# Performance work log

Hardware: AMD Instinct MI355X
Metric: run time of the kernel (lower is better)

## Reference

```python
import jax, jax.numpy as jnp
import numpy as np
from jax import lax

B, C_IN, C_OUT, K, N_W, L = 32, 256, 256, 7, 8, 4096
SQ = C_IN // 32  # squeezed dim = 8
STRIDE, PAD = 1, 3


def setup_inputs() -> dict:
    key = jax.random.key(0)
    ks = jax.random.split(key, 8)
    s = 0.05
    return {
        "x": jax.random.normal(ks[0], (B, C_IN, L), dtype=jnp.float32),
        "conv_weight": jax.random.normal(ks[1], (C_OUT, C_IN, K, N_W), dtype=jnp.float32) * s,
        "w1": jax.random.normal(ks[2], (C_IN, SQ), dtype=jnp.float32) * s,   # linear1 weight (x @ w1)
        "b1": jax.random.normal(ks[3], (SQ,), dtype=jnp.float32) * s,
        "wk": jax.random.normal(ks[4], (SQ, K), dtype=jnp.float32) * s,      # kernel head
        "wi": jax.random.normal(ks[5], (SQ, C_IN), dtype=jnp.float32) * s,   # inc head
        "wo": jax.random.normal(ks[6], (SQ, C_OUT), dtype=jnp.float32) * s,  # outc head
        "wn": jax.random.normal(ks[7], (SQ, N_W), dtype=jnp.float32) * s,    # nums head
    }


def reference(x, conv_weight, w1, b1, wk, wi, wo, wn):
    # SqueezeFeedForward: AdaptiveAvgPool1d(1) == mean over length, then Linear + exact GELU
    pooled = jnp.mean(x, axis=-1)                        # [B, C_in]
    h = jax.nn.gelu(pooled @ w1 + b1, approximate=False)  # [B, SQ]

    kr = jax.nn.sigmoid(h @ wk)          # [B, K]
    inc = jax.nn.sigmoid(h @ wi)         # [B, C_in]
    outc = jax.nn.sigmoid(h @ wo)        # [B, C_out]
    nums = jax.nn.softmax(h @ wn, -1)    # [B, N_w]

    # Per-sample mixed weights: sum over num_weight of 4-way outer-product gated base weight
    w = jnp.einsum('bk,bi,bo,bn,oikn->boik', kr, inc, outc, nums, conv_weight)  # [B,O,I,K]

    b, o, i, k = w.shape
    l = x.shape[-1]
    # Batched per-sample conv via grouped conv: groups = B
    lhs = x.reshape(1, b * i, l)         # [1, B*I, L]
    rhs = w.reshape(b * o, i, k)         # [B*O, I, K]
    out = lax.conv_general_dilated(
        lhs, rhs,
        window_strides=(STRIDE,),
        padding=[(PAD, PAD)],
        dimension_numbers=('NCH', 'OIH', 'NCH'),
        feature_group_count=b,
    )
    return out.reshape(b, o, -1)         # [B, O, L_out]
```

## Files before the change

### kernel.cpp

```cpp
#include <hip/hip_runtime.h>
#include <hip/hip_bf16.h>
#include <math.h>

#define B_   32
#define CI   256
#define CO   256
#define KW   7
#define NW   8
#define SQD  8
#define L_   4096

typedef __attribute__((ext_vector_type(8))) __bf16 bf16x8;
typedef __attribute__((ext_vector_type(4))) __bf16 bf16x4;
typedef __attribute__((ext_vector_type(4))) float  f32x4;

static __device__ __forceinline__ unsigned short f2bf(float f) {
    unsigned int u = __builtin_bit_cast(unsigned int, f);
    u += 0x7FFFu + ((u >> 16) & 1u);
    return (unsigned short)(u >> 16);
}
static __device__ __forceinline__ uint2 pack4bf(float a, float b, float c, float d) {
    bf16x4 v;
    v[0] = (__bf16)a; v[1] = (__bf16)b; v[2] = (__bf16)c; v[3] = (__bf16)d;
    return __builtin_bit_cast(uint2, v);
}

__global__ __launch_bounds__(256) void k1_mean(
        const float* __restrict__ x, float* __restrict__ pooled) {
    int row = blockIdx.x;
    const float* p = x + (size_t)row * L_;
    int t = threadIdx.x;
    float s = 0.f;
#pragma unroll
    for (int it = 0; it < 4; ++it) {
        float4 v = *(const float4*)(p + (size_t)(t + 256 * it) * 4);
        s += v.x + v.y + v.z + v.w;
    }
    for (int m = 1; m <= 32; m <<= 1) s += __shfl_xor(s, m);
    __shared__ float wsum[4];
    if ((t & 63) == 0) wsum[t >> 6] = s;
    __syncthreads();
    if (t == 0)
        pooled[row] = (wsum[0] + wsum[1] + wsum[2] + wsum[3]) * (1.0f / L_);
}

__global__ __launch_bounds__(64) void k2_gates(
        const float* __restrict__ pooled,
        const float* __restrict__ w1, const float* __restrict__ b1,
        const float* __restrict__ wk, const float* __restrict__ wi,
        const float* __restrict__ wo, const float* __restrict__ wn,
        float* __restrict__ kr, float* __restrict__ inc,
        float* __restrict__ outc, float* __restrict__ nums)
{
    int b = blockIdx.x, lane = threadIdx.x;
    float pc[4];
#pragma unroll
    for (int j = 0; j < 4; ++j)
        pc[j] = pooled[b * CI + lane + 64 * j];
    float h[SQD];
#pragma unroll
    for (int s = 0; s < SQD; ++s) {
        float ps = 0.f;
#pragma unroll
        for (int j = 0; j < 4; ++j)
            ps += pc[j] * w1[(lane + 64 * j) * SQD + s];
        for (int m = 1; m <= 32; m <<= 1) ps += __shfl_xor(ps, m);
        float z = ps + b1[s];
        h[s] = 0.5f * z * (1.0f + erff(z * 0.70710678118654752f));
    }
    if (lane < KW) {
        float a = 0.f;
#pragma unroll
        for (int s = 0; s < SQD; ++s) a += h[s] * wk[s * KW + lane];
        kr[b * 8 + lane] = 1.0f / (1.0f + expf(-a));
    }
    if (lane < NW) {
        float e[NW]; float mx = -1e30f;
#pragma unroll
        for (int n = 0; n < NW; ++n) {
            float a = 0.f;
#pragma unroll
            for (int s = 0; s < SQD; ++s) a += h[s] * wn[s * NW + n];
            e[n] = a; mx = fmaxf(mx, a);
        }
        float den = 0.f;
#pragma unroll
        for (int n = 0; n < NW; ++n) den += expf(e[n] - mx);
        nums[b * NW + lane] = expf(e[lane] - mx) / den;
    }
#pragma unroll
    for (int j = 0; j < 4; ++j) {
        int c = lane + 64 * j;
        float a = 0.f, o2 = 0.f;
#pragma unroll
        for (int s = 0; s < SQD; ++s) {
            a  += h[s] * wi[s * CI + c];
            o2 += h[s] * wo[s * CO + c];
        }
        inc[b * CI + c]  = 1.0f / (1.0f + expf(-a));
        outc[b * CO + c] = 1.0f / (1.0f + expf(-o2));
    }
}

__global__ __launch_bounds__(256) void k3_wgen(
        const float* __restrict__ cw,
        const float* __restrict__ kr, const float* __restrict__ inc,
        const float* __restrict__ outc, const float* __restrict__ nums,
        unsigned short* __restrict__ W2) {
    __shared__ float s_nums[B_][NW];
    __shared__ float s_kr[B_][KW];
    __shared__ float s_inc[B_][32];
    __shared__ float s_outc[B_][8];
    int t = threadIdx.x;
    int ic = blockIdx.x & 7, o0 = (blockIdx.x >> 3) * 8;
    s_nums[t >> 3][t & 7] = nums[t];
    if (t < B_ * KW) s_kr[t / KW][t % KW] = kr[(t / KW) * 8 + (t % KW)];
    for (int u = t; u < 32 * 32; u += 256) {
        int bb = u >> 5, ii = u & 31;
        s_inc[bb][ii] = inc[bb * CI + ic * 32 + ii];
    }
    for (int u = t; u < 32 * 8; u += 256) {
        int bb = u >> 3, oo = u & 7;
        s_outc[bb][oo] = outc[bb * CO + o0 + oo];
    }
    __syncthreads();
    int ii = t & 31, oo = t >> 5;
    int o = o0 + oo, i = ic * 32 + ii;
    float cwv[KW][NW];
    const float* p = cw + ((size_t)(o * CI + i)) * (KW * NW);
#pragma unroll
    for (int k = 0; k < KW; ++k)
#pragma unroll
        for (int n = 0; n < NW; ++n) cwv[k][n] = p[k * NW + n];
    for (int bb = 0; bb < B_; ++bb) {
        float gio = s_inc[bb][ii] * s_outc[bb][oo];
#pragma unroll
        for (int k = 0; k < KW; ++k) {
            float sk = 0.f;
#pragma unroll
            for (int n = 0; n < NW; ++n) sk += s_nums[bb][n] * cwv[k][n];
            float w = s_kr[bb][k] * gio * sk;
            W2[(((size_t)(bb * KW + k) * 8 + ic) * CO + o) * 32 + ii] = f2bf(w);
        }
    }
}

__global__ __launch_bounds__(1024) void k4_conv(
        const float* __restrict__ x,
        const unsigned short* __restrict__ W2,
        float* __restrict__ out) {
    __shared__ __align__(16) unsigned short xs[262 * 264];
    int bid = blockIdx.x;
    int wg  = (bid & 7) * 64 + (bid >> 3);
    int b = wg >> 4, l0 = (wg & 15) * 256;
    int t = threadIdx.x;
    const float* xb = x + (size_t)b * CI * L_;

    {
        int P = t >> 4, lam = t & 15;
        int up = P & 31, half = P >> 5;
        int i0 = (up & 7) * 32 + (up >> 3) * 8;
#pragma unroll
        for (int it = 0; it < 2; ++it) {
            int ch = lam + 16 * (half * 2 + it);
            const float* src = xb + (size_t)i0 * L_ + l0 + ch * 4;
            float4 f[8];
#pragma unroll
            for (int e = 0; e < 8; ++e)
                f[e] = *(const float4*)(src + (size_t)e * L_);
#pragma unroll
            for (int j = 0; j < 4; ++j) {
                int r = 4 * ch + j + 3;
                uint2 a = pack4bf((&f[0].x)[j], (&f[1].x)[j], (&f[2].x)[j], (&f[3].x)[j]);
                uint2 c = pack4bf((&f[4].x)[j], (&f[5].x)[j], (&f[6].x)[j], (&f[7].x)[j]);
                uint4 w; w.x = a.x; w.y = a.y; w.z = c.x; w.w = c.y;
                *(uint4*)(xs + r * 264 + up * 8) = w;
            }
        }
    }
    if (t < 128) {
        bool left = t < 64;
        int tt = left ? t : t - 64;
        int i0 = tt * 4;
        int gl4 = left ? l0 - 4 : l0 + 256;
        bool ok = left ? (l0 > 0) : (l0 + 256 < L_);
        float4 f[4];
#pragma unroll
        for (int d = 0; d < 4; ++d)
            f[d] = ok ? *(const float4*)(xb + (size_t)(i0 + d) * L_ + gl4)
                      : make_float4(0.f, 0.f, 0.f, 0.f);
        int eo = ((tt >> 1) & 3) * 64 + (tt >> 3) * 8 + (tt & 1) * 4;
#pragma unroll
        for (int j = 0; j < 4; ++j) {
            if (left && j == 0) continue;
            if (!left && j == 3) continue;
            int r = left ? (j - 1) : (259 + j);
            uint2 w = pack4bf((&f[0].x)[j], (&f[1].x)[j], (&f[2].x)[j], (&f[3].x)[j]);
            *(uint2*)(xs + r * 264 + eo) = w;
        }
    }
    __syncthreads();

    int lane = t & 63, wid = t >> 6;
    int o_base = (wid & 3) * 64;
    int l_wave = (wid >> 2) * 64;
    int ml = lane & 15, kg = lane >> 4;

    f32x4 acc[4][4];
#pragma unroll
    for (int a = 0; a < 4; ++a)
#pragma unroll
        for (int c = 0; c < 4; ++c) acc[a][c] = (f32x4){0.f, 0.f, 0.f, 0.f};

    const unsigned short* wA = W2 + (size_t)b * (56 * CO * 32)
                               + (o_base + ml) * 32 + kg * 8;
    const unsigned short* xB = xs + (l_wave + ml) * 264 + kg * 64;

    for (int k = 0; k < KW; ++k) {
#pragma unroll
        for (int icc = 0; icc < 8; ++icc) {
            int S = k * 8 + icc;
            bf16x8 AF[4], BF[4];
#pragma unroll
            for (int mt = 0; mt < 4; ++mt)
                AF[mt] = *(const bf16x8*)(wA + (size_t)S * (CO * 32) + mt * 16 * 32);
#pragma unroll
            for (int nt = 0; nt < 4; ++nt)
                BF[nt] = *(const bf16x8*)(xB + (nt * 16 + k) * 264 + icc * 8);
            __builtin_amdgcn_s_setprio(1);
#pragma unroll
            for (int mt = 0; mt < 4; ++mt)
#pragma unroll
                for (int nt = 0; nt < 4; ++nt)
                    acc[mt][nt] = __builtin_amdgcn_mfma_f32_16x16x32_bf16(
                        AF[mt], BF[nt], acc[mt][nt], 0, 0, 0);
            __builtin_amdgcn_s_setprio(0);
        }
    }

#pragma unroll
    for (int mt = 0; mt < 4; ++mt) {
        int o = o_base + mt * 16 + kg * 4;
#pragma unroll
        for (int nt = 0; nt < 4; ++nt) {
            int l = l0 + l_wave + nt * 16 + ml;
            float* po = out + ((size_t)(b * CO + o)) * L_ + l;
#pragma unroll
            for (int q = 0; q < 4; ++q)
                po[(size_t)q * L_] = acc[mt][nt][q];
        }
    }
}

extern "C" void kernel_launch(void* const* d_in, const int* in_sizes, int n_in,
                              void* d_out, int out_size, void* d_ws, size_t ws_size,
                              hipStream_t stream) {
    const float* x  = (const float*)d_in[0];
    const float* cw = (const float*)d_in[1];
    const float* w1 = (const float*)d_in[2];
    const float* b1 = (const float*)d_in[3];
    const float* wk = (const float*)d_in[4];
    const float* wi = (const float*)d_in[5];
    const float* wo = (const float*)d_in[6];
    const float* wn = (const float*)d_in[7];
    float* out = (float*)d_out;

    char* ws = (char*)d_ws;
    unsigned short* W2 = (unsigned short*)(ws + 0);
    float* pooled = (float*)(ws + 29360128);
    float* kr     = (float*)(ws + 29392896);
    float* inc    = (float*)(ws + 29393920);
    float* outc   = (float*)(ws + 29426688);
    float* nums   = (float*)(ws + 29459456);

    k1_mean<<<B_ * CI, 256, 0, stream>>>(x, pooled);
    k2_gates<<<B_, 64, 0, stream>>>(pooled, w1, b1, wk, wi, wo, wn,
                                    kr, inc, outc, nums);
    k3_wgen<<<256, 256, 0, stream>>>(cw, kr, inc, outc, nums, W2);
    k4_conv<<<512, 1024, 0, stream>>>(x, W2, out);
}
```

Before: 192.2 us.

## Halve conv tile length to 128 with 512-thread blocks and simpler channel layout

```diff
diff --git a/kernel.cpp b/kernel.cpp
--- a/kernel.cpp
+++ b/kernel.cpp
@@ -145,24 +145,24 @@
     }
 }
 
-__global__ __launch_bounds__(1024) void k4_conv(
+__global__ __launch_bounds__(512, 4) void k4_conv(
         const float* __restrict__ x,
         const unsigned short* __restrict__ W2,
         float* __restrict__ out) {
-    __shared__ __align__(16) unsigned short xs[262 * 264];
+    __shared__ __align__(16) unsigned short xs[134 * 264];
     int bid = blockIdx.x;
-    int wg  = (bid & 7) * 64 + (bid >> 3);
-    int b = wg >> 4, l0 = (wg & 15) * 256;
+    int wg  = (bid & 7) * 128 + (bid >> 3);
+    int b = wg >> 5, l0 = (wg & 31) * 128;
     int t = threadIdx.x;
     const float* xb = x + (size_t)b * CI * L_;
 
     {
-        int P = t >> 4, lam = t & 15;
-        int up = P & 31, half = P >> 5;
-        int i0 = (up & 7) * 32 + (up >> 3) * 8;
+        int u = t >> 4;
+        int lam = t & 15;
+        int i0 = u * 8;
 #pragma unroll
         for (int it = 0; it < 2; ++it) {
-            int ch = lam + 16 * (half * 2 + it);
+            int ch = lam + 16 * it;
             const float* src = xb + (size_t)i0 * L_ + l0 + ch * 4;
             float4 f[8];
 #pragma unroll
@@ -170,34 +170,27 @@
                 f[e] = *(const float4*)(src + (size_t)e * L_);
 #pragma unroll
             for (int j = 0; j < 4; ++j) {
-                int r = 4 * ch + j + 3;
+                int r = ch * 4 + j + 3;
                 uint2 a = pack4bf((&f[0].x)[j], (&f[1].x)[j], (&f[2].x)[j], (&f[3].x)[j]);
                 uint2 c = pack4bf((&f[4].x)[j], (&f[5].x)[j], (&f[6].x)[j], (&f[7].x)[j]);
                 uint4 w; w.x = a.x; w.y = a.y; w.z = c.x; w.w = c.y;
-                *(uint4*)(xs + r * 264 + up * 8) = w;
+                *(uint4*)(xs + r * 264 + u * 8) = w;
             }
         }
     }
-    if (t < 128) {
-        bool left = t < 64;
-        int tt = left ? t : t - 64;
-        int i0 = tt * 4;
-        int gl4 = left ? l0 - 4 : l0 + 256;
-        bool ok = left ? (l0 > 0) : (l0 + 256 < L_);
-        float4 f[4];
-#pragma unroll
-        for (int d = 0; d < 4; ++d)
-            f[d] = ok ? *(const float4*)(xb + (size_t)(i0 + d) * L_ + gl4)
-                      : make_float4(0.f, 0.f, 0.f, 0.f);
-        int eo = ((tt >> 1) & 3) * 64 + (tt >> 3) * 8 + (tt & 1) * 4;
-#pragma unroll
-        for (int j = 0; j < 4; ++j) {
-            if (left && j == 0) continue;
-            if (!left && j == 3) continue;
-            int r = left ? (j - 1) : (259 + j);
-            uint2 w = pack4bf((&f[0].x)[j], (&f[1].x)[j], (&f[2].x)[j], (&f[3].x)[j]);
-            *(uint2*)(xs + r * 264 + eo) = w;
-        }
+    if (t < 192) {
+        int h = t >> 5, u = t & 31;
+        int r = (h < 3) ? h : (128 + h);
+        int gl = l0 - 3 + r;
+        bool ok = (gl >= 0 && gl < L_);
+        float f[8];
+#pragma unroll
+        for (int e = 0; e < 8; ++e)
+            f[e] = ok ? xb[(size_t)(u * 8 + e) * L_ + gl] : 0.f;
+        uint2 a = pack4bf(f[0], f[1], f[2], f[3]);
+        uint2 c = pack4bf(f[4], f[5], f[6], f[7]);
+        uint4 w; w.x = a.x; w.y = a.y; w.z = c.x; w.w = c.y;
+        *(uint4*)(xs + r * 264 + u * 8) = w;
     }
     __syncthreads();
 
@@ -214,7 +207,7 @@
 
     const unsigned short* wA = W2 + (size_t)b * (56 * CO * 32)
                                + (o_base + ml) * 32 + kg * 8;
-    const unsigned short* xB = xs + (l_wave + ml) * 264 + kg * 64;
+    const unsigned short* xB = xs + (l_wave + ml) * 264 + kg * 8;
 
     for (int k = 0; k < KW; ++k) {
 #pragma unroll
@@ -226,7 +219,7 @@
                 AF[mt] = *(const bf16x8*)(wA + (size_t)S * (CO * 32) + mt * 16 * 32);
 #pragma unroll
             for (int nt = 0; nt < 4; ++nt)
-                BF[nt] = *(const bf16x8*)(xB + (nt * 16 + k) * 264 + icc * 8);
+                BF[nt] = *(const bf16x8*)(xB + (nt * 16 + k) * 264 + icc * 32);
             __builtin_amdgcn_s_setprio(1);
 #pragma unroll
             for (int mt = 0; mt < 4; ++mt)
@@ -277,5 +270,5 @@
     k2_gates<<<B_, 64, 0, stream>>>(pooled, w1, b1, wk, wi, wo, wn,
                                     kr, inc, outc, nums);
     k3_wgen<<<256, 256, 0, stream>>>(cw, kr, inc, outc, nums, W2);
-    k4_conv<<<512, 1024, 0, stream>>>(x, W2, out);
-}
+    k4_conv<<<1024, 512, 0, stream>>>(x, W2, out);
+}
```

After: 190.9 us. About the same (-0.7%).
